# Optimization experiments

Hardware: AMD Instinct MI355X
Metric: run time of the kernel (lower is better)

Reference implementation:

```python
import jax, jax.numpy as jnp
import numpy as np

B, V, C, M, CM, D, OUT = 16, 16, 64, 32, 16, 128, 600
VOCAB = {"cond": 4000, "proc": 2000, "drug": 600, "lab_item": 700, "lab_value": 2000, "inj_item": 400, "inj_value": 2000}


def _gru(x, Wih, Whh, bih, bhh):
    """Batch-first torch-style GRU. x: [N,T,D] -> (outputs [N,T,D], h_T [N,D])."""
    Dh = Whh.shape[1]

    def step(h, xt):
        gi = xt @ Wih.T + bih
        gh = h @ Whh.T + bhh
        ir, iz, ig = jnp.split(gi, 3, axis=-1)
        hr, hz, hg = jnp.split(gh, 3, axis=-1)
        r = jax.nn.sigmoid(ir + hr)
        z = jax.nn.sigmoid(iz + hz)
        n = jnp.tanh(ig + r * hg)
        h = (1.0 - z) * n + z * h
        return h, h

    h0 = jnp.zeros((x.shape[0], Dh), x.dtype)
    hT, ys = jax.lax.scan(step, h0, jnp.swapaxes(x, 0, 1))
    return jnp.swapaxes(ys, 0, 1), hT


def _hetero_mp(feats, Wself, Wmsg):
    """Heterogeneous message passing over node types on the fully-connected
    monitor<->visit-feature bipartite pattern: each node type combines a self
    transform with a transformed mean of the other node types, then ReLU.
    feats: list of [N,D]; Wself/Wmsg: [T,D,D]."""
    stacked = jnp.stack(feats)  # [T,N,D]
    total = jnp.sum(stacked, axis=0)
    T = stacked.shape[0]
    outs = []
    for t in range(T):
        others = (total - stacked[t]) / (T - 1)
        outs.append(jax.nn.relu(stacked[t] @ Wself[t] + others @ Wmsg[t]))
    return outs


def _forward(codes_cond, codes_proc, codes_drug, codes_lab_item, codes_lab_value,
             codes_inj_item, codes_inj_value, weight, age,
             emb_cond, emb_proc, emb_drug, emb_lab_item, emb_lab_value,
             emb_inj_item, emb_inj_value,
             mgru_Wih, mgru_Whh, mgru_bih, mgru_bhh,
             vgru_Wih, vgru_Whh, vgru_bih, vgru_bhh,
             gnn_Wself, gnn_Wmsg,
             fc_weight_W, fc_weight_b, fc_age_W, fc_age_b,
             fc_patient_W, fc_patient_b):
    # ---- visit-event features: embedding lookup + sum-pool over codes ----
    vis = {}
    for k, codes, emb in (("cond", codes_cond, emb_cond),
                          ("proc", codes_proc, emb_proc),
                          ("drug", codes_drug, emb_drug)):
        vis[k] = jnp.sum(emb[codes], axis=2)  # [B,V,D]
    visit_keys = ("cond", "proc", "drug")

    # ---- monitor-event pairs: (item * value) embeddings, GNN, two-level GRU ----
    pairs = (
        (codes_lab_item, codes_lab_value, emb_lab_item, emb_lab_value, "lab_item", (0, 2, 3, 4)),
        (codes_inj_item, codes_inj_value, emb_inj_item, emb_inj_value, "inj_item", (1, 2, 3, 4)),
    )
    hid = {}
    for p, (ci, cv, ei, ev, ikey, gidx) in enumerate(pairs):
        mon = jnp.sum(ei[ci] * ev[cv], axis=3)  # [B,V,M,D]
        feats = [mon.reshape(-1, D)]  # monitor node type, [B*V*M, D]
        for k in visit_keys:  # visit features repeated across monitors
            feats.append(jnp.broadcast_to(vis[k][:, :, None, :], (B, V, M, D)).reshape(-1, D))
        outs = _hetero_mp(feats, gnn_Wself[p], gnn_Wmsg[p])
        for t, k in enumerate((ikey,) + visit_keys):
            g = gidx[t]
            # monitor-level GRU over the M monitors of each visit
            o, _ = _gru(outs[t].reshape(B * V, M, D), mgru_Wih[g], mgru_Whh[g], mgru_bih[g], mgru_bhh[g])
            last = o[:, -1, :].reshape(B, V, D)  # last monitor state per visit
            # visit-level GRU (source uses visit_gru[feature_key1] for all keys)
            _, h = _gru(last, vgru_Wih[p], vgru_Whh[p], vgru_bih[p], vgru_bhh[p])
            hid[k] = h if k not in hid else hid[k] + h

    # ---- weight / age scalar features ----
    for k, x, W, b, vi in (("weight", weight, fc_weight_W, fc_weight_b, 2),
                           ("age", age, fc_age_W, fc_age_b, 3)):
        mask = (x != 0.0)[..., None]  # [B,V,1]
        xe = (x[..., None] * W[:, 0] + b) * mask  # Linear(1->D) then zero-mask
        _, h = _gru(xe, vgru_Wih[vi], vgru_Whh[vi], vgru_bih[vi], vgru_bhh[vi])
        hid[k] = h

    # ---- concat in dict-insertion order, then ReLU + Linear head ----
    pe = jnp.concatenate([hid["lab_item"], hid["cond"], hid["proc"], hid["drug"],
                          hid["inj_item"], hid["weight"], hid["age"]], axis=-1)  # [B, 7D]
    return jax.nn.relu(pe) @ fc_patient_W.T + fc_patient_b  # [B, OUT]


def setup_inputs() -> dict:
    key = jax.random.key(0)
    ks = iter(jax.random.split(key, 64))

    def nrm(shape, s=0.1):
        return (jax.random.normal(next(ks), shape) * s).astype(jnp.float32)

    def emb_table(vsz):
        t = nrm((vsz, D), 1.0)
        return t.at[0].set(0.0)  # padding_idx=0 row is zero

    inp = {}
    inp["codes_cond"] = jax.random.randint(next(ks), (B, V, C), 0, VOCAB["cond"], dtype=jnp.int32)
    inp["codes_proc"] = jax.random.randint(next(ks), (B, V, C), 0, VOCAB["proc"], dtype=jnp.int32)
    inp["codes_drug"] = jax.random.randint(next(ks), (B, V, C), 0, VOCAB["drug"], dtype=jnp.int32)
    inp["codes_lab_item"] = jax.random.randint(next(ks), (B, V, M, CM), 0, VOCAB["lab_item"], dtype=jnp.int32)
    inp["codes_lab_value"] = jax.random.randint(next(ks), (B, V, M, CM), 0, VOCAB["lab_value"], dtype=jnp.int32)
    inp["codes_inj_item"] = jax.random.randint(next(ks), (B, V, M, CM), 0, VOCAB["inj_item"], dtype=jnp.int32)
    inp["codes_inj_value"] = jax.random.randint(next(ks), (B, V, M, CM), 0, VOCAB["inj_value"], dtype=jnp.int32)
    inp["weight"] = jax.random.uniform(next(ks), (B, V), minval=0.1, maxval=1.0, dtype=jnp.float32)
    inp["age"] = jax.random.uniform(next(ks), (B, V), minval=0.1, maxval=1.0, dtype=jnp.float32)
    inp["emb_cond"] = emb_table(VOCAB["cond"])
    inp["emb_proc"] = emb_table(VOCAB["proc"])
    inp["emb_drug"] = emb_table(VOCAB["drug"])
    inp["emb_lab_item"] = emb_table(VOCAB["lab_item"])
    inp["emb_lab_value"] = emb_table(VOCAB["lab_value"])
    inp["emb_inj_item"] = emb_table(VOCAB["inj_item"])
    inp["emb_inj_value"] = emb_table(VOCAB["inj_value"])
    inp["mgru_Wih"] = nrm((5, 3 * D, D))
    inp["mgru_Whh"] = nrm((5, 3 * D, D))
    inp["mgru_bih"] = nrm((5, 3 * D))
    inp["mgru_bhh"] = nrm((5, 3 * D))
    inp["vgru_Wih"] = nrm((4, 3 * D, D))
    inp["vgru_Whh"] = nrm((4, 3 * D, D))
    inp["vgru_bih"] = nrm((4, 3 * D))
    inp["vgru_bhh"] = nrm((4, 3 * D))
    inp["gnn_Wself"] = nrm((2, 4, D, D))
    inp["gnn_Wmsg"] = nrm((2, 4, D, D))
    inp["fc_weight_W"] = nrm((D, 1))
    inp["fc_weight_b"] = nrm((D,))
    inp["fc_age_W"] = nrm((D, 1))
    inp["fc_age_b"] = nrm((D,))
    inp["fc_patient_W"] = nrm((OUT, 7 * D))
    inp["fc_patient_b"] = nrm((OUT,))
    return inp


def reference(codes_cond, codes_proc, codes_drug, codes_lab_item, codes_lab_value,
              codes_inj_item, codes_inj_value, weight, age,
              emb_cond, emb_proc, emb_drug, emb_lab_item, emb_lab_value,
              emb_inj_item, emb_inj_value,
              mgru_Wih, mgru_Whh, mgru_bih, mgru_bhh,
              vgru_Wih, vgru_Whh, vgru_bih, vgru_bhh,
              gnn_Wself, gnn_Wmsg,
              fc_weight_W, fc_weight_b, fc_age_W, fc_age_b,
              fc_patient_W, fc_patient_b):
    return _forward(codes_cond, codes_proc, codes_drug, codes_lab_item, codes_lab_value,
                    codes_inj_item, codes_inj_value, weight, age,
                    emb_cond, emb_proc, emb_drug, emb_lab_item, emb_lab_value,
                    emb_inj_item, emb_inj_value,
                    mgru_Wih, mgru_Whh, mgru_bih, mgru_bhh,
                    vgru_Wih, vgru_Whh, vgru_bih, vgru_bhh,
                    gnn_Wself, gnn_Wmsg,
                    fc_weight_W, fc_weight_b, fc_age_W, fc_age_b,
                    fc_patient_W, fc_patient_b)
```

## Files before the change

kernel.cpp:

```cpp
#include <hip/hip_runtime.h>
#include <math.h>

#define B_   16
#define V_   16
#define C_   64
#define M_   32
#define CM_  16
#define D_   128
#define OUT_ 600
#define NSEQ 256
#define NROW 8192

typedef __attribute__((ext_vector_type(8))) short bf16x8;
typedef __attribute__((ext_vector_type(4))) short bf16x4;
typedef __attribute__((ext_vector_type(4))) float f32x4;

__device__ __forceinline__ unsigned short f2bf(float x) {
  union { float f; unsigned u; } v; v.f = x;
  unsigned r = v.u + 0x7fff + ((v.u >> 16) & 1);
  return (unsigned short)(r >> 16);
}
__device__ __forceinline__ float bf2f(short s) {
  union { unsigned u; float f; } v;
  v.u = ((unsigned)(unsigned short)s) << 16;
  return v.f;
}
__device__ __forceinline__ float fsig(float x)  { return __fdividef(1.f, 1.f + __expf(-x)); }
__device__ __forceinline__ float ftanh(float x) { return 1.f - 2.f*__fdividef(1.f, __expf(2.f*x) + 1.f); }

__device__ __forceinline__ void ldsbar() {
  asm volatile("s_waitcnt lgkmcnt(0)" ::: "memory");
  __builtin_amdgcn_s_barrier();
  asm volatile("" ::: "memory");
}

constexpr int OFF_VIS   = 0;
constexpr int OFF_VISB  = 98304;
constexpr int OFF_MONB  = 147456;
constexpr int OFF_TOTB  = 1196032;
constexpr int OFF_W12T  = 2244608;
constexpr int OFF_WIHB  = 2375680;
constexpr int OFF_WIHTV = 2498560;
constexpr int OFF_XE    = 2695168;
constexpr int OFF_LAST  = 27926528;
constexpr int OFF_VH    = 29171712;

__global__ __launch_bounds__(256) void k_prepvis(
    const float* __restrict__ Wself, const float* __restrict__ Wmsg,
    const float* __restrict__ mWih,  const float* __restrict__ vWih,
    const float* __restrict__ wgt,   const float* __restrict__ age,
    const float* __restrict__ fwW,   const float* __restrict__ fwB,
    const float* __restrict__ faW,   const float* __restrict__ faB,
    const int* __restrict__ cc, const int* __restrict__ cp, const int* __restrict__ cd,
    const float* __restrict__ ec, const float* __restrict__ ep, const float* __restrict__ ed,
    short* __restrict__ w12t, short* __restrict__ wihb,
    float* __restrict__ wihTv, float* __restrict__ xe,
    float* __restrict__ vis, short* __restrict__ visb)
{
  int bx = blockIdx.x, tid = threadIdx.x;
  if (bx < 1024) {
    int lin = bx*256 + tid;
    int pt = lin >> 15, rem = lin & 32767;
    int n = rem >> 8, k = rem & 255;
    float v;
    if (k < 128) v = Wself[pt*16384 + k*128 + n] - Wmsg[pt*16384 + k*128 + n]*(1.f/3.f);
    else         v = Wmsg[pt*16384 + (k-128)*128 + n]*(1.f/3.f);
    w12t[lin] = (short)f2bf(v);
  } else if (bx < 1984) {
    int lin = (bx-1024)*256 + tid;
    wihb[lin] = (short)f2bf(mWih[lin]);
  } else if (bx < 2752) {
    int lin = (bx-1984)*256 + tid;
    int g = lin / 49152, rem2 = lin % 49152;
    int k = rem2 / 384, j = rem2 % 384;
    wihTv[lin] = vWih[g*49152 + j*128 + k];
  } else if (bx < 3008) {
    int lin = (bx-2752)*256 + tid;
    int which = lin >> 15, rem2 = lin & 32767;
    int n = rem2 >> 7, d = rem2 & 127;
    float x  = which ? age[n] : wgt[n];
    float Wv = which ? faW[d] : fwW[d];
    float bb = which ? faB[d] : fwB[d];
    xe[lin] = (x != 0.0f) ? (x*Wv + bb) : 0.0f;
  } else {
    int idx = (bx-3008)*256 + tid;
    int type = idx >> 15;
    int r = idx & 32767;
    int bv = r >> 7, d = r & 127;
    const int*   codes = (type==0) ? cc : (type==1) ? cp : cd;
    const float* emb   = (type==0) ? ec : (type==1) ? ep : ed;
    float acc = 0.f;
    for (int c = 0; c < C_; ++c) {
      int code = codes[bv*C_ + c];
      acc += emb[code*D_ + d];
    }
    vis [(type*NSEQ + bv)*D_ + d] = acc;
    visb[(type*NSEQ + bv)*D_ + d] = (short)f2bf(acc);
  }
}

__global__ __launch_bounds__(128) void k_mon(
    const int* __restrict__ cli, const int* __restrict__ clv,
    const int* __restrict__ cii, const int* __restrict__ civ,
    const float* __restrict__ eli, const float* __restrict__ elv,
    const float* __restrict__ eii, const float* __restrict__ eiv,
    const float* __restrict__ vis,
    short* __restrict__ monb, short* __restrict__ totb)
{
  int p   = blockIdx.x >> 13;
  int bvm = blockIdx.x & 8191;
  int d   = threadIdx.x;
  const int* ci = p ? cii : cli;  const int* cv = p ? civ : clv;
  const float* ei = p ? eii : eli; const float* ev = p ? eiv : elv;
  float acc = 0.f;
  #pragma unroll
  for (int c = 0; c < CM_; ++c) {
    int iv = ci[bvm*CM_ + c];
    int vv = cv[bvm*CM_ + c];
    acc += ei[iv*D_ + d] * ev[vv*D_ + d];
  }
  int bv = bvm >> 5;
  float vsum = vis[bv*D_ + d] + vis[(NSEQ + bv)*D_ + d] + vis[(2*NSEQ + bv)*D_ + d];
  monb[(p*NROW + bvm)*D_ + d] = (short)f2bf(acc);
  totb[(p*NROW + bvm)*D_ + d] = (short)f2bf(acc + vsum);
}

__global__ __launch_bounds__(512, 1) void k_ggru(
    const short* __restrict__ monb, const short* __restrict__ totb,
    const short* __restrict__ visb, const short* __restrict__ w12t,
    const short* __restrict__ wihb, const float* __restrict__ mWhh,
    const float* __restrict__ mbih, const float* __restrict__ mbhh,
    float* __restrict__ last)
{
  const int run  = blockIdx.x >> 4;
  const int pair = blockIdx.x & 15;
  const int p = run >> 2, t = run & 3;
  const int g = (run % 4 == 0) ? (run / 4) : (run % 4 + 1);
  const int tid = threadIdx.x;
  const int w = tid >> 6;
  const int lane = tid & 63;
  const int c = lane & 15, q = lane >> 4;
  const int j = w*16 + c;

  __shared__ short hb[2][4][16][40];
  __shared__ __align__(16) short Ys[2][16][136];
  __shared__ __align__(16) short Xl[2][4096];

  for (int idx = tid; idx < 2*4*16*40; idx += 512)
    ((short*)hb)[idx] = 0;

  bf16x8 bW12[8];
  #pragma unroll
  for (int kt = 0; kt < 8; ++kt)
    bW12[kt] = *(const bf16x8*)(w12t + (size_t)run*32768 + (size_t)(w*16+c)*256 + kt*32 + q*8);

  bf16x8 bWih[3][4];
  #pragma unroll
  for (int gate = 0; gate < 3; ++gate)
    #pragma unroll
    for (int kt = 0; kt < 4; ++kt)
      bWih[gate][kt] = *(const bf16x8*)(wihb + ((size_t)g*384 + gate*128 + j)*128 + kt*32 + q*8);

  bf16x8 bWhh[3][4];
  #pragma unroll
  for (int gate = 0; gate < 3; ++gate) {
    const float* wp = mWhh + ((size_t)g*384 + gate*128 + j)*128 + q*8;
    #pragma unroll
    for (int kt = 0; kt < 4; ++kt) {
      float4 lo = *(const float4*)(wp + kt*32);
      float4 hi = *(const float4*)(wp + kt*32 + 4);
      bf16x8 tt;
      tt[0]=(short)f2bf(lo.x); tt[1]=(short)f2bf(lo.y); tt[2]=(short)f2bf(lo.z); tt[3]=(short)f2bf(lo.w);
      tt[4]=(short)f2bf(hi.x); tt[5]=(short)f2bf(hi.y); tt[6]=(short)f2bf(hi.z); tt[7]=(short)f2bf(hi.w);
      bWhh[gate][kt] = tt;
    }
  }
  const float bs0 = mbih[g*384 +       j] + mbhh[g*384 +       j];
  const float bs1 = mbih[g*384 + 128 + j] + mbhh[g*384 + 128 + j];
  const float bi2 = mbih[g*384 + 256 + j];
  const float bh2 = mbhh[g*384 + 256 + j];

  const int xr_ = tid >> 5, xu = tid & 31;
  const int bv = pair*16 + xr_;
  const short* fsrc;
  int fstride;
  if (xu < 16) {
    if (t == 0) { fsrc = monb + ((size_t)p*NROW + (size_t)bv*32)*128 + xu*8; fstride = 128; }
    else        { fsrc = visb + ((size_t)(t-1)*NSEQ + bv)*128 + xu*8;        fstride = 0;   }
  } else {
    fsrc = totb + ((size_t)p*NROW + (size_t)bv*32)*128 + (xu-16)*8;          fstride = 128;
  }
  const int xdofs = xr_*256 + (((xu*16) ^ ((xr_&7)<<4)) >> 1);
  short* xdst0 = &Xl[0][xdofs];
  short* xdst1 = &Xl[1][xdofs];

  {
    bf16x8 x0 = *(const bf16x8*)fsrc;
    bf16x8 x1 = *(const bf16x8*)(fsrc + fstride);
    *(bf16x8*)xdst0 = x0;
    *(bf16x8*)xdst1 = x1;
  }
  float hf[4] = {0.f,0.f,0.f,0.f};
  const int ktw = w >> 1;
  const int kkw = (w & 1)*16 + c;
  ldsbar();

  {
    const char* xbase = (const char*)&Xl[0][0];
    f32x4 accY = (f32x4){0.f,0.f,0.f,0.f};
    #pragma unroll
    for (int kt = 0; kt < 8; ++kt) {
      bf16x8 aX = *(const bf16x8*)(xbase + c*512 + ((kt*64 + q*16) ^ ((c&7)<<4)));
      accY = __builtin_amdgcn_mfma_f32_16x16x32_bf16(aX, bW12[kt], accY, 0, 0, 0);
    }
    #pragma unroll
    for (int reg = 0; reg < 4; ++reg)
      Ys[0][q*4 + reg][w*16 + c] = (short)f2bf(fmaxf(accY[reg], 0.f));
  }
  ldsbar();

  #pragma unroll 1
  for (int m = 0; m < 32; ++m) {
    const int cur = m & 1, nxt = cur ^ 1;

    bf16x8 xnext;
    if (m < 30) xnext = *(const bf16x8*)(fsrc + (size_t)(m+2)*fstride);

    f32x4 accY = (f32x4){0.f,0.f,0.f,0.f};
    if (m < 31) {
      const char* xbase = (const char*)&Xl[nxt][0];
      #pragma unroll
      for (int kt = 0; kt < 8; ++kt) {
        bf16x8 aX = *(const bf16x8*)(xbase + c*512 + ((kt*64 + q*16) ^ ((c&7)<<4)));
        accY = __builtin_amdgcn_mfma_f32_16x16x32_bf16(aX, bW12[kt], accY, 0, 0, 0);
      }
    }

    bf16x8 ah[4], a2[4];
    #pragma unroll
    for (int kt = 0; kt < 4; ++kt) {
      ah[kt] = *(const bf16x8*)&hb[cur][kt][c][q*8];
      a2[kt] = *(const bf16x8*)&Ys[cur][c][kt*32 + q*8];
    }
    f32x4 acc0 = (f32x4){0.f,0.f,0.f,0.f};
    f32x4 acc1 = (f32x4){0.f,0.f,0.f,0.f};
    f32x4 aG2  = (f32x4){0.f,0.f,0.f,0.f};
    f32x4 aH2  = (f32x4){0.f,0.f,0.f,0.f};
    #pragma unroll
    for (int kt = 0; kt < 4; ++kt) {
      acc0 = __builtin_amdgcn_mfma_f32_16x16x32_bf16(ah[kt], bWhh[0][kt], acc0, 0, 0, 0);
      acc1 = __builtin_amdgcn_mfma_f32_16x16x32_bf16(ah[kt], bWhh[1][kt], acc1, 0, 0, 0);
      aH2  = __builtin_amdgcn_mfma_f32_16x16x32_bf16(ah[kt], bWhh[2][kt], aH2,  0, 0, 0);
    }
    #pragma unroll
    for (int kt = 0; kt < 4; ++kt) {
      acc0 = __builtin_amdgcn_mfma_f32_16x16x32_bf16(a2[kt], bWih[0][kt], acc0, 0, 0, 0);
      acc1 = __builtin_amdgcn_mfma_f32_16x16x32_bf16(a2[kt], bWih[1][kt], acc1, 0, 0, 0);
      aG2  = __builtin_amdgcn_mfma_f32_16x16x32_bf16(a2[kt], bWih[2][kt], aG2,  0, 0, 0);
    }

    if (m < 31) {
      #pragma unroll
      for (int reg = 0; reg < 4; ++reg)
        Ys[nxt][q*4 + reg][w*16 + c] = (short)f2bf(fmaxf(accY[reg], 0.f));
    }
    if (m < 30) *(bf16x8*)(cur ? xdst1 : xdst0) = xnext;

    #pragma unroll
    for (int reg = 0; reg < 4; ++reg) {
      float rr = fsig(acc0[reg] + bs0);
      float zz = fsig(acc1[reg] + bs1);
      float nn = ftanh(aG2[reg] + bi2 + rr*(aH2[reg] + bh2));
      float hnew = (1.f - zz)*nn + zz*hf[reg];
      hf[reg] = hnew;
      hb[nxt][ktw][q*4 + reg][kkw] = (short)f2bf(hnew);
    }
    ldsbar();
  }

  #pragma unroll
  for (int reg = 0; reg < 4; ++reg)
    last[((size_t)run*NSEQ + pair*16 + q*4 + reg)*D_ + j] = hf[reg];
}

__global__ __launch_bounds__(768) void k_vgru(
    const float* __restrict__ last, const float* __restrict__ xe,
    const float* __restrict__ wihTv, const float* __restrict__ vbih,
    const float* __restrict__ vWhh, const float* __restrict__ vbhh,
    float* __restrict__ vh)
{
  int run = blockIdx.x >> 4, b = blockIdx.x & 15;
  int tid = threadIdx.x;
  int vidx = (run < 4) ? 0 : (run < 8) ? 1 : (run - 6);

  __shared__ float Xs[16][128];
  __shared__ float giL[16*384];
  __shared__ __align__(16) float hsv[128];
  __shared__ float gh[384];

  const float* X = (run < 8) ? (last + ((size_t)run*NSEQ + b*16)*D_)
                             : (xe + ((size_t)(run-8)*NSEQ + b*16)*D_);
  for (int idx = tid; idx < 2048; idx += 768)
    ((float*)Xs)[idx] = X[idx];
  if (tid < 128) hsv[tid] = 0.f;
  __syncthreads();

  {
    int half = (tid >= 384) ? 1 : 0;
    int j = tid - half*384;
    float accv[8];
    float bias = vbih[vidx*384 + j];
    #pragma unroll
    for (int s = 0; s < 8; ++s) accv[s] = bias;
    const float* W = wihTv + vidx*49152 + j;
    #pragma unroll 4
    for (int k = 0; k < 128; ++k) {
      float wv = W[k*384];
      #pragma unroll
      for (int s = 0; s < 8; ++s) accv[s] += Xs[half*8 + s][k] * wv;
    }
    #pragma unroll
    for (int s = 0; s < 8; ++s)
      giL[(half*8 + s)*384 + j] = accv[s];
  }

  int j = tid >> 1, kh = tid & 1;
  float w[64];
  const float4* wrow = (const float4*)(vWhh + (vidx*384 + j)*128 + kh*64);
  #pragma unroll
  for (int k4 = 0; k4 < 16; ++k4) {
    float4 t4 = wrow[k4];
    w[4*k4] = t4.x; w[4*k4+1] = t4.y; w[4*k4+2] = t4.z; w[4*k4+3] = t4.w;
  }
  float bj = vbhh[vidx*384 + j];
  __syncthreads();

  #pragma unroll 1
  for (int v = 0; v < 16; ++v) {
    const float4* h4 = (const float4*)(hsv + kh*64);
    float p0 = 0.f, p1 = 0.f;
    #pragma unroll
    for (int k4 = 0; k4 < 8; ++k4) {
      float4 u0 = h4[k4], u1 = h4[k4+8];
      p0 += w[4*k4   ]*u0.x + w[4*k4+1 ]*u0.y + w[4*k4+2 ]*u0.z + w[4*k4+3 ]*u0.w;
      p1 += w[4*k4+32]*u1.x + w[4*k4+33]*u1.y + w[4*k4+34]*u1.z + w[4*k4+35]*u1.w;
    }
    float part = p0 + p1;
    part += __shfl_xor(part, 1);
    if (kh == 0) gh[j] = bj + ((j < 256) ? giL[v*384 + j] : 0.f) + part;
    __syncthreads();
    if (tid < 128) {
      float r = fsig(gh[tid]);
      float z = fsig(gh[tid+128]);
      float gin = giL[v*384 + 256 + tid];
      float n = ftanh(gin + r*gh[tid+256]);
      hsv[tid] = (1.f - z)*n + z*hsv[tid];
    }
    __syncthreads();
  }
  if (tid < 128) vh[(run*16 + b)*D_ + tid] = hsv[tid];
}

__global__ __launch_bounds__(256) void k_head(
    const float* __restrict__ vh, const float* __restrict__ Wp,
    const float* __restrict__ bp, float* __restrict__ out)
{
  const int o = blockIdx.x;
  const int tid = threadIdx.x;
  const int b = tid & 15, kc = tid >> 4;
  const int a1[7] = {0,1,2,3,4,8,9};
  const int a2[7] = {-1,5,6,7,-1,-1,-1};
  const float4* wb = (const float4*)(Wp + (size_t)o*896 + kc*56);
  float acc = 0.f;
  #pragma unroll
  for (int i = 0; i < 14; ++i) {
    int cc2 = kc*56 + i*4;
    int s = cc2 >> 7, d0 = cc2 & 127;
    float4 a = *(const float4*)(vh + (a1[s]*16 + b)*D_ + d0);
    int s2 = a2[s];
    if (s2 >= 0) {
      float4 a2v = *(const float4*)(vh + (s2*16 + b)*D_ + d0);
      a.x += a2v.x; a.y += a2v.y; a.z += a2v.z; a.w += a2v.w;
    }
    a.x = fmaxf(a.x, 0.f); a.y = fmaxf(a.y, 0.f);
    a.z = fmaxf(a.z, 0.f); a.w = fmaxf(a.w, 0.f);
    float4 ww = wb[i];
    acc += a.x*ww.x + a.y*ww.y + a.z*ww.z + a.w*ww.w;
  }
  __shared__ float red[16][17];
  red[kc][b] = acc;
  __syncthreads();
  if (tid < 16) {
    float s = 0.f;
    #pragma unroll
    for (int k = 0; k < 16; ++k) s += red[k][tid];
    out[tid*OUT_ + o] = s + bp[o];
  }
}

extern "C" void kernel_launch(void* const* d_in, const int* in_sizes, int n_in,
                              void* d_out, int out_size, void* d_ws, size_t ws_size,
                              hipStream_t stream)
{
  (void)in_sizes; (void)n_in; (void)out_size; (void)ws_size;
  const int*   cc   = (const int*)  d_in[0];
  const int*   cp   = (const int*)  d_in[1];
  const int*   cd   = (const int*)  d_in[2];
  const int*   cli  = (const int*)  d_in[3];
  const int*   clv  = (const int*)  d_in[4];
  const int*   cii  = (const int*)  d_in[5];
  const int*   civ  = (const int*)  d_in[6];
  const float* wgt  = (const float*)d_in[7];
  const float* age  = (const float*)d_in[8];
  const float* ec   = (const float*)d_in[9];
  const float* ep   = (const float*)d_in[10];
  const float* ed   = (const float*)d_in[11];
  const float* eli  = (const float*)d_in[12];
  const float* elv  = (const float*)d_in[13];
  const float* eii  = (const float*)d_in[14];
  const float* eiv  = (const float*)d_in[15];
  const float* mWih = (const float*)d_in[16];
  const float* mWhh = (const float*)d_in[17];
  const float* mbih = (const float*)d_in[18];
  const float* mbhh = (const float*)d_in[19];
  const float* vWih = (const float*)d_in[20];
  const float* vWhh = (const float*)d_in[21];
  const float* vbih = (const float*)d_in[22];
  const float* vbhh = (const float*)d_in[23];
  const float* Wself= (const float*)d_in[24];
  const float* Wmsg = (const float*)d_in[25];
  const float* fwW  = (const float*)d_in[26];
  const float* fwB  = (const float*)d_in[27];
  const float* faW  = (const float*)d_in[28];
  const float* faB  = (const float*)d_in[29];
  const float* Wp   = (const float*)d_in[30];
  const float* bp   = (const float*)d_in[31];
  float* out = (float*)d_out;
  float* ws  = (float*)d_ws;

  float* vis   = ws + OFF_VIS;
  short* visb  = (short*)(ws + OFF_VISB);
  short* monb  = (short*)(ws + OFF_MONB);
  short* totb  = (short*)(ws + OFF_TOTB);
  short* w12t  = (short*)(ws + OFF_W12T);
  short* wihb  = (short*)(ws + OFF_WIHB);
  float* wihTv = ws + OFF_WIHTV;
  float* xe    = ws + OFF_XE;
  float* last  = ws + OFF_LAST;
  float* vh    = ws + OFF_VH;

  k_prepvis<<<3392, 256, 0, stream>>>(Wself, Wmsg, mWih, vWih, wgt, age,
                                      fwW, fwB, faW, faB,
                                      cc, cp, cd, ec, ep, ed,
                                      w12t, wihb, wihTv, xe, vis, visb);
  k_mon <<<16384, 128, 0, stream>>>(cli, clv, cii, civ, eli, elv, eii, eiv,
                                    vis, monb, totb);
  k_ggru<<<128, 512, 0, stream>>>(monb, totb, visb, w12t, wihb,
                                  mWhh, mbih, mbhh, last);
  k_vgru<<<160, 768, 0, stream>>>(last, xe, wihTv, vbih, vWhh, vbhh, vh);
  k_head<<<600, 256, 0, stream>>>(vh, Wp, bp, out);
}
```

Baseline: 248.2 us.

## Fuse monitor pooling into prep kernel and compute totals inside GRU

Merges the monitor embedding-product pooling into the prep kernel so it runs in the same launch as the visit pooling, removing one kernel launch. It also drops the separate totb buffer and its fp32 vis copy: the GRU kernel now adds the three visit sums to the monitor rows on the fly while staging inputs. This cuts global writes and reads of a large bf16 buffer. In exchange it adds per-step conversion work inside the serial GRU loop and introduces double bf16 rounding on the total input.

```diff
diff --git a/kernel.cpp b/kernel.cpp
--- a/kernel.cpp
+++ b/kernel.cpp
@@ -34,10 +34,8 @@
   asm volatile("" ::: "memory");
 }
 
-constexpr int OFF_VIS   = 0;
 constexpr int OFF_VISB  = 98304;
 constexpr int OFF_MONB  = 147456;
-constexpr int OFF_TOTB  = 1196032;
 constexpr int OFF_W12T  = 2244608;
 constexpr int OFF_WIHB  = 2375680;
 constexpr int OFF_WIHTV = 2498560;
@@ -53,9 +51,13 @@
     const float* __restrict__ faW,   const float* __restrict__ faB,
     const int* __restrict__ cc, const int* __restrict__ cp, const int* __restrict__ cd,
     const float* __restrict__ ec, const float* __restrict__ ep, const float* __restrict__ ed,
+    const int* __restrict__ cli, const int* __restrict__ clv,
+    const int* __restrict__ cii, const int* __restrict__ civ,
+    const float* __restrict__ eli, const float* __restrict__ elv,
+    const float* __restrict__ eii, const float* __restrict__ eiv,
     short* __restrict__ w12t, short* __restrict__ wihb,
     float* __restrict__ wihTv, float* __restrict__ xe,
-    float* __restrict__ vis, short* __restrict__ visb)
+    short* __restrict__ visb, short* __restrict__ monb)
 {
   int bx = blockIdx.x, tid = threadIdx.x;
   if (bx < 1024) {
@@ -82,7 +84,7 @@
     float Wv = which ? faW[d] : fwW[d];
     float bb = which ? faB[d] : fwB[d];
     xe[lin] = (x != 0.0f) ? (x*Wv + bb) : 0.0f;
-  } else {
+  } else if (bx < 3392) {
     int idx = (bx-3008)*256 + tid;
     int type = idx >> 15;
     int r = idx & 32767;
@@ -94,43 +96,29 @@
       int code = codes[bv*C_ + c];
       acc += emb[code*D_ + d];
     }
-    vis [(type*NSEQ + bv)*D_ + d] = acc;
     visb[(type*NSEQ + bv)*D_ + d] = (short)f2bf(acc);
-  }
-}
-
-__global__ __launch_bounds__(128) void k_mon(
-    const int* __restrict__ cli, const int* __restrict__ clv,
-    const int* __restrict__ cii, const int* __restrict__ civ,
-    const float* __restrict__ eli, const float* __restrict__ elv,
-    const float* __restrict__ eii, const float* __restrict__ eiv,
-    const float* __restrict__ vis,
-    short* __restrict__ monb, short* __restrict__ totb)
-{
-  int p   = blockIdx.x >> 13;
-  int bvm = blockIdx.x & 8191;
-  int d   = threadIdx.x;
-  const int* ci = p ? cii : cli;  const int* cv = p ? civ : clv;
-  const float* ei = p ? eii : eli; const float* ev = p ? eiv : elv;
-  float acc = 0.f;
-  #pragma unroll
-  for (int c = 0; c < CM_; ++c) {
-    int iv = ci[bvm*CM_ + c];
-    int vv = cv[bvm*CM_ + c];
-    acc += ei[iv*D_ + d] * ev[vv*D_ + d];
-  }
-  int bv = bvm >> 5;
-  float vsum = vis[bv*D_ + d] + vis[(NSEQ + bv)*D_ + d] + vis[(2*NSEQ + bv)*D_ + d];
-  monb[(p*NROW + bvm)*D_ + d] = (short)f2bf(acc);
-  totb[(p*NROW + bvm)*D_ + d] = (short)f2bf(acc + vsum);
+  } else {
+    int rowid = (bx-3392)*2 + (tid >> 7);
+    int p = rowid >> 13, bvm = rowid & 8191;
+    int d = tid & 127;
+    const int* ci = p ? cii : cli;  const int* cv = p ? civ : clv;
+    const float* ei = p ? eii : eli; const float* ev = p ? eiv : elv;
+    float acc = 0.f;
+    #pragma unroll
+    for (int c2 = 0; c2 < CM_; ++c2) {
+      int iv = ci[bvm*CM_ + c2];
+      int vv = cv[bvm*CM_ + c2];
+      acc += ei[iv*D_ + d] * ev[vv*D_ + d];
+    }
+    monb[((size_t)p*NROW + bvm)*D_ + d] = (short)f2bf(acc);
+  }
 }
 
 __global__ __launch_bounds__(512, 1) void k_ggru(
-    const short* __restrict__ monb, const short* __restrict__ totb,
-    const short* __restrict__ visb, const short* __restrict__ w12t,
-    const short* __restrict__ wihb, const float* __restrict__ mWhh,
-    const float* __restrict__ mbih, const float* __restrict__ mbhh,
-    float* __restrict__ last)
+    const short* __restrict__ monb, const short* __restrict__ visb,
+    const short* __restrict__ w12t, const short* __restrict__ wihb,
+    const float* __restrict__ mWhh, const float* __restrict__ mbih,
+    const float* __restrict__ mbhh, float* __restrict__ last)
 {
   const int run  = blockIdx.x >> 4;
   const int pair = blockIdx.x & 15;
@@ -182,21 +170,35 @@
 
   const int xr_ = tid >> 5, xu = tid & 31;
   const int bv = pair*16 + xr_;
+  const bool istot = (xu >= 16);
   const short* fsrc;
   int fstride;
-  if (xu < 16) {
+  float vsf[8] = {0.f,0.f,0.f,0.f,0.f,0.f,0.f,0.f};
+  if (!istot) {
     if (t == 0) { fsrc = monb + ((size_t)p*NROW + (size_t)bv*32)*128 + xu*8; fstride = 128; }
     else        { fsrc = visb + ((size_t)(t-1)*NSEQ + bv)*128 + xu*8;        fstride = 0;   }
   } else {
-    fsrc = totb + ((size_t)p*NROW + (size_t)bv*32)*128 + (xu-16)*8;          fstride = 128;
-  }
+    fsrc = monb + ((size_t)p*NROW + (size_t)bv*32)*128 + (xu-16)*8;          fstride = 128;
+    #pragma unroll
+    for (int i = 0; i < 8; ++i)
+      vsf[i] = bf2f(visb[(0*NSEQ + bv)*128 + (xu-16)*8 + i])
+             + bf2f(visb[(1*NSEQ + bv)*128 + (xu-16)*8 + i])
+             + bf2f(visb[(2*NSEQ + bv)*128 + (xu-16)*8 + i]);
+  }
+  auto fixtot = [&](bf16x8 x) -> bf16x8 {
+    if (istot) {
+      #pragma unroll
+      for (int i = 0; i < 8; ++i) x[i] = (short)f2bf(bf2f(x[i]) + vsf[i]);
+    }
+    return x;
+  };
   const int xdofs = xr_*256 + (((xu*16) ^ ((xr_&7)<<4)) >> 1);
   short* xdst0 = &Xl[0][xdofs];
   short* xdst1 = &Xl[1][xdofs];
 
   {
-    bf16x8 x0 = *(const bf16x8*)fsrc;
-    bf16x8 x1 = *(const bf16x8*)(fsrc + fstride);
+    bf16x8 x0 = fixtot(*(const bf16x8*)fsrc);
+    bf16x8 x1 = fixtot(*(const bf16x8*)(fsrc + fstride));
     *(bf16x8*)xdst0 = x0;
     *(bf16x8*)xdst1 = x1;
   }
@@ -264,7 +266,7 @@
       for (int reg = 0; reg < 4; ++reg)
         Ys[nxt][q*4 + reg][w*16 + c] = (short)f2bf(fmaxf(accY[reg], 0.f));
     }
-    if (m < 30) *(bf16x8*)(cur ? xdst1 : xdst0) = xnext;
+    if (m < 30) *(bf16x8*)(cur ? xdst1 : xdst0) = fixtot(xnext);
 
     #pragma unroll
     for (int reg = 0; reg < 4; ++reg) {
@@ -438,10 +440,8 @@
   float* out = (float*)d_out;
   float* ws  = (float*)d_ws;
 
-  float* vis   = ws + OFF_VIS;
   short* visb  = (short*)(ws + OFF_VISB);
   short* monb  = (short*)(ws + OFF_MONB);
-  short* totb  = (short*)(ws + OFF_TOTB);
   short* w12t  = (short*)(ws + OFF_W12T);
   short* wihb  = (short*)(ws + OFF_WIHB);
   float* wihTv = ws + OFF_WIHTV;
@@ -449,13 +449,12 @@
   float* last  = ws + OFF_LAST;
   float* vh    = ws + OFF_VH;
 
-  k_prepvis<<<3392, 256, 0, stream>>>(Wself, Wmsg, mWih, vWih, wgt, age,
-                                      fwW, fwB, faW, faB,
-                                      cc, cp, cd, ec, ep, ed,
-                                      w12t, wihb, wihTv, xe, vis, visb);
-  k_mon <<<16384, 128, 0, stream>>>(cli, clv, cii, civ, eli, elv, eii, eiv,
-                                    vis, monb, totb);
-  k_ggru<<<128, 512, 0, stream>>>(monb, totb, visb, w12t, wihb,
+  k_prepvis<<<11584, 256, 0, stream>>>(Wself, Wmsg, mWih, vWih, wgt, age,
+                                       fwW, fwB, faW, faB,
+                                       cc, cp, cd, ec, ep, ed,
+                                       cli, clv, cii, civ, eli, elv, eii, eiv,
+                                       w12t, wihb, wihTv, xe, visb, monb);
+  k_ggru<<<128, 512, 0, stream>>>(monb, visb, w12t, wihb,
                                   mWhh, mbih, mbhh, last);
   k_vgru<<<160, 768, 0, stream>>>(last, xe, wihTv, vbih, vWhh, vbhh, vh);
   k_head<<<600, 256, 0, stream>>>(vh, Wp, bp, out);
```

New measurement: 251.3 us. Within noise of the previous version (+1.2%).
